# Performance work log

Measured on AMD Instinct MI355X. Metric: run time of the kernel, lower is better.

The kernel has to match this reference:

```python
import jax, jax.numpy as jnp
import numpy as np

N = 50000      # num nodes
IN = 256       # in_channels
H = 4          # heads
C = 64         # out_channels per head (concat=False -> out_dim = C)
HOPS = 3       # max_hops == num hops provided
E = 400000     # edges per hop
NEG_SLOPE = 0.2


def setup_inputs() -> dict:
    key = jax.random.key(0)
    ks = jax.random.split(key, 10)
    s_in = 1.0 / np.sqrt(IN)
    s_c = 1.0 / np.sqrt(C)
    return {
        "x": jax.random.normal(ks[0], (N, IN), jnp.float32),
        "ei0": jax.random.randint(ks[1], (2, E), 0, N, dtype=jnp.int32),
        "ei1": jax.random.randint(ks[2], (2, E), 0, N, dtype=jnp.int32),
        "ei2": jax.random.randint(ks[3], (2, E), 0, N, dtype=jnp.int32),
        # shared left/right projections (lin_l / lin_r, shared across hops)
        "W_l": jax.random.normal(ks[4], (IN, H * C), jnp.float32) * s_in,
        "b_l": jnp.zeros((H * C,), jnp.float32),
        "W_r": jax.random.normal(ks[5], (IN, H * C), jnp.float32) * s_in,
        "b_r": jnp.zeros((H * C,), jnp.float32),
        # hop-specific attention vectors and output biases
        "att": jax.random.normal(ks[6], (HOPS, H, C), jnp.float32) * s_c,
        "bias": jnp.zeros((HOPS, C), jnp.float32),
        # hop gate (single Linear since gate_hidden=None)
        "W_gate": jax.random.normal(ks[7], (IN, HOPS), jnp.float32) * s_in,
        "b_gate": jnp.zeros((HOPS,), jnp.float32),
    }


def _segment_softmax(logits, seg, n):
    # logits: [E, H], seg: [E] destination node ids
    m = jax.ops.segment_max(logits, seg, num_segments=n)          # [N, H]
    m = jnp.where(jnp.isfinite(m), m, 0.0)                        # empty segments -> 0
    ex = jnp.exp(logits - m[seg])
    s = jax.ops.segment_sum(ex, seg, num_segments=n)              # [N, H]
    return ex / (s[seg] + 1e-16)


def _gatv2_hop(x_l, x_r, edge_index, att_k, bias_k):
    # x_l, x_r: [N, H, C] shared projections; edge_index: [2, Ek]
    src, dst = edge_index[0], edge_index[1]
    s = jax.nn.leaky_relu(x_l[src] + x_r[dst], NEG_SLOPE)         # [Ek, H, C]
    alpha = jnp.einsum("ehc,hc->eh", s, att_k)                    # [Ek, H]
    alpha = _segment_softmax(alpha, dst, N)
    msg = jax.ops.segment_sum(x_l[src] * alpha[..., None], dst, num_segments=N)  # [N, H, C]
    return msg.mean(axis=1) + bias_k                              # concat=False -> head mean, [N, C]


def reference(x, ei0, ei1, ei2, W_l, b_l, W_r, b_r, att, bias, W_gate, b_gate):
    # shared projections computed once
    x_l = (x @ W_l + b_l).reshape(N, H, C)
    x_r = (x @ W_r + b_r).reshape(N, H, C)

    # hop 0 gets self-loops (add_self_loops=True); higher hops do not
    ar = jnp.arange(N, dtype=ei0.dtype)
    ei0_sl = jnp.concatenate([ei0, jnp.stack([ar, ar])], axis=1)
    edges = [ei0_sl, ei1, ei2]

    messages = jnp.stack(
        [_gatv2_hop(x_l, x_r, edges[k], att[k], bias[k]) for k in range(HOPS)],
        axis=1,
    )  # [N, HOPS, C]

    logits = x @ W_gate + b_gate                                  # [N, HOPS]
    weights = jax.nn.softmax(logits, axis=-1)
    out = jnp.einsum("nkc,nk->nc", messages, weights)             # [N, C]
    return out
```

## Files before the change

### kernel.cpp

```cpp
#include <hip/hip_runtime.h>
#include <math.h>

#define N_NODES 50000
#define IN_DIM 256
#define HEADS 4
#define CDIM 64
#define HC 256
#define HOPS 3
#define EDGES 400000
#define NEG_SLOPE 0.2f
#define SEG (EDGES + N_NODES)
#define TOT_E (3 * EDGES + N_NODES)
#define CAP 40

#define NB_GATE  ((N_NODES + 3) / 4)
#define NB_PACKW ((IN_DIM * 2 * HC) / 256)
#define NB_SCAT  ((TOT_E + 255) / 256)
#define GEMM_BX  ((N_NODES + 127) / 128)

typedef unsigned short ushort;
using short8  = __attribute__((ext_vector_type(8))) short;
using floatx4 = __attribute__((ext_vector_type(4))) float;

__device__ __forceinline__ void decode_flat(int f, int& k, int& e)
{
    if (f < SEG)              { k = 0; e = f; }
    else if (f < SEG + EDGES) { k = 1; e = f - SEG; }
    else                      { k = 2; e = f - SEG - EDGES; }
}

__device__ __forceinline__ ushort f2bf(float f)
{
    unsigned u = __float_as_uint(f);
    unsigned r = u + 0x7fffu + ((u >> 16) & 1u);
    return (ushort)(r >> 16);
}

__global__ __launch_bounds__(256) void prep(
    const float* __restrict__ X, const float* __restrict__ Wg,
    const float* __restrict__ bg, float* __restrict__ gw,
    ushort* __restrict__ Xb,
    const float* __restrict__ Wl, const float* __restrict__ Wr,
    ushort* __restrict__ WT,
    const int* __restrict__ ei0, const int* __restrict__ ei1,
    const int* __restrict__ ei2, int* __restrict__ cnt,
    int* __restrict__ bucket)
{
    const int blk = blockIdx.x;
    const int tid = threadIdx.x;

    if (blk < NB_GATE) {
        const int node = (blk * 256 + tid) >> 6;
        const int lane = tid & 63;
        if (node >= N_NODES) return;

        float4 xv = ((const float4*)(X + (size_t)node * IN_DIM))[lane];

        union { ushort s[4]; uint2 u; } o;
        o.s[0] = f2bf(xv.x); o.s[1] = f2bf(xv.y);
        o.s[2] = f2bf(xv.z); o.s[3] = f2bf(xv.w);
        ((uint2*)(Xb + (size_t)node * IN_DIM))[lane] = o.u;

        float a0 = 0.f, a1 = 0.f, a2 = 0.f;
        const int i0 = lane * 4;
        a0 += xv.x * Wg[(i0 + 0) * HOPS + 0]; a1 += xv.x * Wg[(i0 + 0) * HOPS + 1]; a2 += xv.x * Wg[(i0 + 0) * HOPS + 2];
        a0 += xv.y * Wg[(i0 + 1) * HOPS + 0]; a1 += xv.y * Wg[(i0 + 1) * HOPS + 1]; a2 += xv.y * Wg[(i0 + 1) * HOPS + 2];
        a0 += xv.z * Wg[(i0 + 2) * HOPS + 0]; a1 += xv.z * Wg[(i0 + 2) * HOPS + 1]; a2 += xv.z * Wg[(i0 + 2) * HOPS + 2];
        a0 += xv.w * Wg[(i0 + 3) * HOPS + 0]; a1 += xv.w * Wg[(i0 + 3) * HOPS + 1]; a2 += xv.w * Wg[(i0 + 3) * HOPS + 2];

        #pragma unroll
        for (int off = 32; off >= 1; off >>= 1) {
            a0 += __shfl_xor(a0, off);
            a1 += __shfl_xor(a1, off);
            a2 += __shfl_xor(a2, off);
        }
        if (lane == 0) {
            float l0 = a0 + bg[0], l1 = a1 + bg[1], l2 = a2 + bg[2];
            float m = fmaxf(l0, fmaxf(l1, l2));
            float e0 = expf(l0 - m), e1 = expf(l1 - m), e2 = expf(l2 - m);
            float inv = 1.f / (e0 + e1 + e2);
            gw[node * HOPS + 0] = e0 * inv;
            gw[node * HOPS + 1] = e1 * inv;
            gw[node * HOPS + 2] = e2 * inv;
        }
    } else if (blk < NB_GATE + NB_PACKW) {
        int id = (blk - NB_GATE) * 256 + tid;
        int n = id >> 8;
        int k = id & 255;
        float v = (n < HC) ? Wl[k * HC + n] : Wr[k * HC + (n - HC)];
        WT[(size_t)n * IN_DIM + k] = f2bf(v);
    } else {
        int f = (blk - NB_GATE - NB_PACKW) * 256 + tid;
        if (f >= TOT_E) return;
        int k, e; decode_flat(f, k, e);
        int s, d;
        if (k == 0 && e >= EDGES) { s = d = e - EDGES; }
        else {
            const int* ei = (k == 0) ? ei0 : (k == 1) ? ei1 : ei2;
            s = ei[e]; d = ei[EDGES + e];
        }
        int pos = atomicAdd(&cnt[k * N_NODES + d], 1);
        if (pos < CAP)
            bucket[((size_t)k * N_NODES + d) * CAP + pos] = s;
    }
}

#define TM 128
#define TN 128
#define TK 32
#define LDP 40

__global__ __launch_bounds__(256) void gemm_mfma(
    const ushort* __restrict__ Xb, const ushort* __restrict__ WT,
    const float* __restrict__ b_l, const float* __restrict__ b_r,
    ushort* __restrict__ xlb, ushort* __restrict__ xrb, int M)
{
    __shared__ ushort As[TM][LDP];
    __shared__ ushort Bs[TN][LDP];
    const int tid  = threadIdx.x;
    const int wave = tid >> 6, lane = tid & 63;
    const int row0 = blockIdx.x * TM;
    const int col0 = blockIdx.y * TN;
    const int wy = (wave >> 1) * 64, wx = (wave & 1) * 64;
    const int lrow = lane & 15, lk = (lane >> 4) * 8;

    floatx4 acc[4][4];
    #pragma unroll
    for (int i = 0; i < 4; i++)
        #pragma unroll
        for (int j = 0; j < 4; j++)
            acc[i][j] = (floatx4){0.f, 0.f, 0.f, 0.f};

    for (int k0 = 0; k0 < IN_DIM; k0 += TK) {
        #pragma unroll
        for (int j = 0; j < 2; j++) {
            int id = tid + 256 * j;
            int r  = id >> 2;
            int c  = (id & 3) * 8;
            int gr = row0 + r;
            uint4 v = make_uint4(0u, 0u, 0u, 0u);
            if (gr < M)
                v = *(const uint4*)(Xb + (size_t)gr * IN_DIM + k0 + c);
            *(uint4*)&As[r][c] = v;
        }
        #pragma unroll
        for (int j = 0; j < 2; j++) {
            int id = tid + 256 * j;
            int r  = id >> 2;
            int c  = (id & 3) * 8;
            *(uint4*)&Bs[r][c] =
                *(const uint4*)(WT + (size_t)(col0 + r) * IN_DIM + k0 + c);
        }
        __syncthreads();

        short8 af[4], bf[4];
        #pragma unroll
        for (int mi = 0; mi < 4; mi++)
            af[mi] = *(const short8*)&As[wy + mi * 16 + lrow][lk];
        #pragma unroll
        for (int ni = 0; ni < 4; ni++)
            bf[ni] = *(const short8*)&Bs[wx + ni * 16 + lrow][lk];

        #pragma unroll
        for (int mi = 0; mi < 4; mi++)
            #pragma unroll
            for (int ni = 0; ni < 4; ni++)
                acc[mi][ni] = __builtin_amdgcn_mfma_f32_16x16x32_bf16(
                    bf[ni], af[mi], acc[mi][ni], 0, 0, 0);
        __syncthreads();
    }

    const int csub = (lane >> 4) * 4;
    #pragma unroll
    for (int mi = 0; mi < 4; mi++) {
        int grow = row0 + wy + mi * 16 + lrow;
        if (grow < M) {
            #pragma unroll
            for (int ni = 0; ni < 4; ni++) {
                int gcol = col0 + wx + ni * 16 + csub;
                floatx4 v = acc[mi][ni];
                const bool left = (gcol < HC);
                const float4 b = left ? *(const float4*)(b_l + gcol)
                                      : *(const float4*)(b_r + gcol - HC);
                union { ushort s[4]; uint2 u; } o;
                o.s[0] = f2bf(v[0] + b.x);
                o.s[1] = f2bf(v[1] + b.y);
                o.s[2] = f2bf(v[2] + b.z);
                o.s[3] = f2bf(v[3] + b.w);
                ushort* dst = left ? (xlb + (size_t)grow * HC + gcol)
                                   : (xrb + (size_t)grow * HC + gcol - HC);
                *(uint2*)dst = o.u;
            }
        }
    }
}

__global__ __launch_bounds__(192) void node_all(
    const ushort* __restrict__ xlb, const ushort* __restrict__ xrb,
    const int* __restrict__ cnt, const int* __restrict__ bucket,
    const float* __restrict__ att, const float* __restrict__ gw,
    const float* __restrict__ bias, float* __restrict__ out)
{
    __shared__ float lds[HOPS][CDIM];
    const int n    = blockIdx.x;
    const int k    = threadIdx.x >> 6;
    const int lane = threadIdx.x & 63;
    const int half = lane >> 5;
    const int sub  = lane & 31;

    const int deg = min(cnt[k * N_NODES + n], CAP);
    const int* bk = bucket + ((size_t)k * N_NODES + n) * CAP;

    uint4 rq = *(const uint4*)(xrb + (size_t)n * HC + sub * 8);
    const float rr0 = __uint_as_float(rq.x << 16);
    const float rr1 = __uint_as_float(rq.x & 0xffff0000u);
    const float rr2 = __uint_as_float(rq.y << 16);
    const float rr3 = __uint_as_float(rq.y & 0xffff0000u);
    const float rr4 = __uint_as_float(rq.z << 16);
    const float rr5 = __uint_as_float(rq.z & 0xffff0000u);
    const float rr6 = __uint_as_float(rq.w << 16);
    const float rr7 = __uint_as_float(rq.w & 0xffff0000u);

    const float4 wa = ((const float4*)(att + (size_t)k * HC))[sub * 2 + 0];
    const float4 wb = ((const float4*)(att + (size_t)k * HC))[sub * 2 + 1];

    float denom = 0.f;
    float acc[8] = {0.f, 0.f, 0.f, 0.f, 0.f, 0.f, 0.f, 0.f};

    if (deg > 0) {
        int myS = (lane < deg) ? bk[lane] : 0;
        const int npair = (deg + 1) >> 1;

        int s0 = __shfl(myS, min(half, deg - 1));
        uint4 q = *(const uint4*)(xlb + (size_t)s0 * HC + sub * 8);

        for (int j = 0; j < npair; j++) {
            int idxn = min(2 * (j + 1) + half, deg - 1);
            int sn = __shfl(myS, idxn);
            uint4 qn = *(const uint4*)(xlb + (size_t)sn * HC + sub * 8);

            float f0 = __uint_as_float(q.x << 16);
            float f1 = __uint_as_float(q.x & 0xffff0000u);
            float f2 = __uint_as_float(q.y << 16);
            float f3 = __uint_as_float(q.y & 0xffff0000u);
            float f4 = __uint_as_float(q.z << 16);
            float f5 = __uint_as_float(q.z & 0xffff0000u);
            float f6 = __uint_as_float(q.w << 16);
            float f7 = __uint_as_float(q.w & 0xffff0000u);

            float v0 = f0 + rr0, v1 = f1 + rr1, v2 = f2 + rr2, v3 = f3 + rr3;
            float v4 = f4 + rr4, v5 = f5 + rr5, v6 = f6 + rr6, v7 = f7 + rr7;

            float p;
            p = 0.6f * wa.x * v0 + 0.4f * wa.x * fabsf(v0);
            p = fmaf(0.6f * wa.y, v1, p); p = fmaf(0.4f * wa.y, fabsf(v1), p);
            p = fmaf(0.6f * wa.z, v2, p); p = fmaf(0.4f * wa.z, fabsf(v2), p);
            p = fmaf(0.6f * wa.w, v3, p); p = fmaf(0.4f * wa.w, fabsf(v3), p);
            p = fmaf(0.6f * wb.x, v4, p); p = fmaf(0.4f * wb.x, fabsf(v4), p);
            p = fmaf(0.6f * wb.y, v5, p); p = fmaf(0.4f * wb.y, fabsf(v5), p);
            p = fmaf(0.6f * wb.z, v6, p); p = fmaf(0.4f * wb.z, fabsf(v6), p);
            p = fmaf(0.6f * wb.w, v7, p); p = fmaf(0.4f * wb.w, fabsf(v7), p);

            p += __shfl_xor(p, 1);
            p += __shfl_xor(p, 2);
            p += __shfl_xor(p, 4);

            bool valid = (2 * j + half) < deg;
            float ex = valid ? __expf(p) : 0.f;
            denom += ex;
            acc[0] = fmaf(ex, f0, acc[0]);
            acc[1] = fmaf(ex, f1, acc[1]);
            acc[2] = fmaf(ex, f2, acc[2]);
            acc[3] = fmaf(ex, f3, acc[3]);
            acc[4] = fmaf(ex, f4, acc[4]);
            acc[5] = fmaf(ex, f5, acc[5]);
            acc[6] = fmaf(ex, f6, acc[6]);
            acc[7] = fmaf(ex, f7, acc[7]);
            q = qn;
        }
    }

    denom += __shfl_xor(denom, 32);
    #pragma unroll
    for (int i = 0; i < 8; i++) acc[i] += __shfl_xor(acc[i], 32);

    float inv = (denom > 0.f) ? 1.f / denom : 0.f;
    const float g  = gw[n * HOPS + k];
    const float* bb = bias + (size_t)k * CDIM + (sub & 7) * 8;

    #pragma unroll
    for (int i = 0; i < 8; i++) {
        float v = acc[i] * inv;
        v += __shfl_xor(v, 8);
        v += __shfl_xor(v, 16);
        if (lane < 8) lds[k][lane * 8 + i] = g * (v * 0.25f + bb[i]);
    }
    __syncthreads();

    if (threadIdx.x < CDIM)
        out[(size_t)n * CDIM + threadIdx.x] =
            lds[0][threadIdx.x] + lds[1][threadIdx.x] + lds[2][threadIdx.x];
}

extern "C" void kernel_launch(void* const* d_in, const int* in_sizes, int n_in,
                              void* d_out, int out_size, void* d_ws, size_t ws_size,
                              hipStream_t stream)
{
    const float* x      = (const float*)d_in[0];
    const int*   ei0    = (const int*)d_in[1];
    const int*   ei1    = (const int*)d_in[2];
    const int*   ei2    = (const int*)d_in[3];
    const float* W_l    = (const float*)d_in[4];
    const float* b_l    = (const float*)d_in[5];
    const float* W_r    = (const float*)d_in[6];
    const float* b_r    = (const float*)d_in[7];
    const float* att    = (const float*)d_in[8];
    const float* bias   = (const float*)d_in[9];
    const float* W_gate = (const float*)d_in[10];
    const float* b_gate = (const float*)d_in[11];

    const size_t NHC = (size_t)N_NODES * HC;
    float* ws      = (float*)d_ws;
    float* gwbuf   = ws;
    int*   cnt     = (int*)(gwbuf + HOPS * N_NODES);
    int*   bucket  = cnt + HOPS * N_NODES;
    ushort* xlb    = (ushort*)(bucket + (size_t)HOPS * N_NODES * CAP);
    ushort* xrb    = xlb + NHC;
    ushort* Xb     = xrb + NHC;
    ushort* WT     = Xb + NHC;

    hipMemsetAsync(cnt, 0, (size_t)HOPS * N_NODES * sizeof(int), stream);

    prep<<<NB_GATE + NB_PACKW + NB_SCAT, 256, 0, stream>>>(
        x, W_gate, b_gate, gwbuf, Xb, W_l, W_r, WT,
        ei0, ei1, ei2, cnt, bucket);

    dim3 ggrid(GEMM_BX, 4);
    gemm_mfma<<<ggrid, 256, 0, stream>>>(Xb, WT, b_l, b_r, xlb, xrb, N_NODES);

    node_all<<<N_NODES, 192, 0, stream>>>(
        xlb, xrb, cnt, bucket, att, gwbuf, bias, (float*)d_out);
}
```

Measured before the change: 393.8 us.

## Process all hops per wave with packed float2 math, drop LDS reduction

The node aggregation kernel now assigns one wave per node and loops over the three hops serially inside that wave. Previously each node got a block of three waves, one per hop, combined through LDS and a barrier. Hop results are accumulated in registers and written directly with vector stores. Leaky-ReLU and the attention dot product are rewritten with packed two-wide float ops and an elementwise max. This removes the LDS and barrier cost and the tiny blocks, but each wave now runs its hops serially, which lowers memory-level parallelism per node.

```diff
diff --git a/kernel.cpp b/kernel.cpp
--- a/kernel.cpp
+++ b/kernel.cpp
@@ -21,6 +21,7 @@
 typedef unsigned short ushort;
 using short8  = __attribute__((ext_vector_type(8))) short;
 using floatx4 = __attribute__((ext_vector_type(4))) float;
+using f32x2   = __attribute__((ext_vector_type(2))) float;
 
 __device__ __forceinline__ void decode_flat(int f, int& k, int& e)
 {
@@ -34,6 +35,19 @@
     unsigned u = __float_as_uint(f);
     unsigned r = u + 0x7fffu + ((u >> 16) & 1u);
     return (ushort)(r >> 16);
+}
+
+__device__ __forceinline__ f32x2 bf2x(unsigned u)
+{
+    f32x2 r;
+    r.x = __uint_as_float(u << 16);
+    r.y = __uint_as_float(u & 0xffff0000u);
+    return r;
+}
+
+__device__ __forceinline__ f32x2 lrelu2(f32x2 v)
+{
+    return __builtin_elementwise_max(v, 0.2f * v);
 }
 
 __global__ __launch_bounds__(256) void prep(
@@ -195,111 +209,107 @@
     }
 }
 
-__global__ __launch_bounds__(192) void node_all(
+__global__ __launch_bounds__(256) void node_all(
     const ushort* __restrict__ xlb, const ushort* __restrict__ xrb,
     const int* __restrict__ cnt, const int* __restrict__ bucket,
     const float* __restrict__ att, const float* __restrict__ gw,
     const float* __restrict__ bias, float* __restrict__ out)
 {
-    __shared__ float lds[HOPS][CDIM];
-    const int n    = blockIdx.x;
-    const int k    = threadIdx.x >> 6;
+    const int n    = blockIdx.x * 4 + (threadIdx.x >> 6);
     const int lane = threadIdx.x & 63;
+    if (n >= N_NODES) return;
     const int half = lane >> 5;
     const int sub  = lane & 31;
-
-    const int deg = min(cnt[k * N_NODES + n], CAP);
-    const int* bk = bucket + ((size_t)k * N_NODES + n) * CAP;
-
-    uint4 rq = *(const uint4*)(xrb + (size_t)n * HC + sub * 8);
-    const float rr0 = __uint_as_float(rq.x << 16);
-    const float rr1 = __uint_as_float(rq.x & 0xffff0000u);
-    const float rr2 = __uint_as_float(rq.y << 16);
-    const float rr3 = __uint_as_float(rq.y & 0xffff0000u);
-    const float rr4 = __uint_as_float(rq.z << 16);
-    const float rr5 = __uint_as_float(rq.z & 0xffff0000u);
-    const float rr6 = __uint_as_float(rq.w << 16);
-    const float rr7 = __uint_as_float(rq.w & 0xffff0000u);
-
-    const float4 wa = ((const float4*)(att + (size_t)k * HC))[sub * 2 + 0];
-    const float4 wb = ((const float4*)(att + (size_t)k * HC))[sub * 2 + 1];
-
-    float denom = 0.f;
-    float acc[8] = {0.f, 0.f, 0.f, 0.f, 0.f, 0.f, 0.f, 0.f};
-
-    if (deg > 0) {
-        int myS = (lane < deg) ? bk[lane] : 0;
-        const int npair = (deg + 1) >> 1;
-
-        int s0 = __shfl(myS, min(half, deg - 1));
-        uint4 q = *(const uint4*)(xlb + (size_t)s0 * HC + sub * 8);
-
-        for (int j = 0; j < npair; j++) {
-            int idxn = min(2 * (j + 1) + half, deg - 1);
-            int sn = __shfl(myS, idxn);
-            uint4 qn = *(const uint4*)(xlb + (size_t)sn * HC + sub * 8);
-
-            float f0 = __uint_as_float(q.x << 16);
-            float f1 = __uint_as_float(q.x & 0xffff0000u);
-            float f2 = __uint_as_float(q.y << 16);
-            float f3 = __uint_as_float(q.y & 0xffff0000u);
-            float f4 = __uint_as_float(q.z << 16);
-            float f5 = __uint_as_float(q.z & 0xffff0000u);
-            float f6 = __uint_as_float(q.w << 16);
-            float f7 = __uint_as_float(q.w & 0xffff0000u);
-
-            float v0 = f0 + rr0, v1 = f1 + rr1, v2 = f2 + rr2, v3 = f3 + rr3;
-            float v4 = f4 + rr4, v5 = f5 + rr5, v6 = f6 + rr6, v7 = f7 + rr7;
-
-            float p;
-            p = 0.6f * wa.x * v0 + 0.4f * wa.x * fabsf(v0);
-            p = fmaf(0.6f * wa.y, v1, p); p = fmaf(0.4f * wa.y, fabsf(v1), p);
-            p = fmaf(0.6f * wa.z, v2, p); p = fmaf(0.4f * wa.z, fabsf(v2), p);
-            p = fmaf(0.6f * wa.w, v3, p); p = fmaf(0.4f * wa.w, fabsf(v3), p);
-            p = fmaf(0.6f * wb.x, v4, p); p = fmaf(0.4f * wb.x, fabsf(v4), p);
-            p = fmaf(0.6f * wb.y, v5, p); p = fmaf(0.4f * wb.y, fabsf(v5), p);
-            p = fmaf(0.6f * wb.z, v6, p); p = fmaf(0.4f * wb.z, fabsf(v6), p);
-            p = fmaf(0.6f * wb.w, v7, p); p = fmaf(0.4f * wb.w, fabsf(v7), p);
-
-            p += __shfl_xor(p, 1);
-            p += __shfl_xor(p, 2);
-            p += __shfl_xor(p, 4);
-
-            bool valid = (2 * j + half) < deg;
-            float ex = valid ? __expf(p) : 0.f;
-            denom += ex;
-            acc[0] = fmaf(ex, f0, acc[0]);
-            acc[1] = fmaf(ex, f1, acc[1]);
-            acc[2] = fmaf(ex, f2, acc[2]);
-            acc[3] = fmaf(ex, f3, acc[3]);
-            acc[4] = fmaf(ex, f4, acc[4]);
-            acc[5] = fmaf(ex, f5, acc[5]);
-            acc[6] = fmaf(ex, f6, acc[6]);
-            acc[7] = fmaf(ex, f7, acc[7]);
-            q = qn;
-        }
-    }
-
-    denom += __shfl_xor(denom, 32);
+    const unsigned laneoff = (unsigned)sub * 8;
+
+    uint4 rq = *(const uint4*)(xrb + (size_t)n * HC + laneoff);
+    f32x2 rr[4] = { bf2x(rq.x), bf2x(rq.y), bf2x(rq.z), bf2x(rq.w) };
+
+    f32x2 outacc[4] = { {0.f,0.f}, {0.f,0.f}, {0.f,0.f}, {0.f,0.f} };
+
     #pragma unroll
-    for (int i = 0; i < 8; i++) acc[i] += __shfl_xor(acc[i], 32);
-
-    float inv = (denom > 0.f) ? 1.f / denom : 0.f;
-    const float g  = gw[n * HOPS + k];
-    const float* bb = bias + (size_t)k * CDIM + (sub & 7) * 8;
-
-    #pragma unroll
-    for (int i = 0; i < 8; i++) {
-        float v = acc[i] * inv;
-        v += __shfl_xor(v, 8);
-        v += __shfl_xor(v, 16);
-        if (lane < 8) lds[k][lane * 8 + i] = g * (v * 0.25f + bb[i]);
-    }
-    __syncthreads();
-
-    if (threadIdx.x < CDIM)
-        out[(size_t)n * CDIM + threadIdx.x] =
-            lds[0][threadIdx.x] + lds[1][threadIdx.x] + lds[2][threadIdx.x];
+    for (int k = 0; k < HOPS; ++k) {
+        const int deg = min(cnt[k * N_NODES + n], CAP);
+        const int* bk = bucket + ((size_t)k * N_NODES + n) * CAP;
+
+        const float4 a0 = ((const float4*)(att + (size_t)k * HC))[sub * 2 + 0];
+        const float4 a1 = ((const float4*)(att + (size_t)k * HC))[sub * 2 + 1];
+        f32x2 w2[4] = { {a0.x, a0.y}, {a0.z, a0.w}, {a1.x, a1.y}, {a1.z, a1.w} };
+
+        float denom = 0.f;
+        f32x2 acc2[4] = { {0.f,0.f}, {0.f,0.f}, {0.f,0.f}, {0.f,0.f} };
+
+        if (deg > 0) {
+            const int degm1 = deg - 1;
+            int myS = (lane < deg) ? bk[lane] : 0;
+            const int npair = (deg + 1) >> 1;
+
+            int s0 = __shfl(myS, min(half, degm1));
+            uint4 q = *(const uint4*)(xlb + (unsigned)s0 * HC + laneoff);
+
+            for (int j = 0; j < npair; j++) {
+                int sn = __shfl(myS, min(2 * (j + 1) + half, degm1));
+                uint4 qn = *(const uint4*)(xlb + (unsigned)sn * HC + laneoff);
+
+                f32x2 f0 = bf2x(q.x), f1 = bf2x(q.y);
+                f32x2 f2 = bf2x(q.z), f3 = bf2x(q.w);
+
+                f32x2 pp = w2[0] * lrelu2(f0 + rr[0]);
+                pp = __builtin_elementwise_fma(w2[1], lrelu2(f1 + rr[1]), pp);
+                pp = __builtin_elementwise_fma(w2[2], lrelu2(f2 + rr[2]), pp);
+                pp = __builtin_elementwise_fma(w2[3], lrelu2(f3 + rr[3]), pp);
+                float p = pp.x + pp.y;
+
+                p += __shfl_xor(p, 1);
+                p += __shfl_xor(p, 2);
+                p += __shfl_xor(p, 4);
+
+                bool valid = (2 * j + half) < deg;
+                float ex = valid ? __expf(p) : 0.f;
+                denom += ex;
+                f32x2 ex2 = { ex, ex };
+                acc2[0] = __builtin_elementwise_fma(ex2, f0, acc2[0]);
+                acc2[1] = __builtin_elementwise_fma(ex2, f1, acc2[1]);
+                acc2[2] = __builtin_elementwise_fma(ex2, f2, acc2[2]);
+                acc2[3] = __builtin_elementwise_fma(ex2, f3, acc2[3]);
+                q = qn;
+            }
+        }
+
+        denom += __shfl_xor(denom, 32);
+        const float inv = (denom > 0.f) ? 1.f / denom : 0.f;
+        #pragma unroll
+        for (int i = 0; i < 4; i++) {
+            acc2[i].x += __shfl_xor(acc2[i].x, 32);
+            acc2[i].y += __shfl_xor(acc2[i].y, 32);
+            acc2[i].x *= inv;
+            acc2[i].y *= inv;
+            acc2[i].x += __shfl_xor(acc2[i].x, 8);
+            acc2[i].y += __shfl_xor(acc2[i].y, 8);
+            acc2[i].x += __shfl_xor(acc2[i].x, 16);
+            acc2[i].y += __shfl_xor(acc2[i].y, 16);
+        }
+
+        const float g   = gw[n * HOPS + k];
+        const float s   = g * 0.25f;
+        const f32x2 s2  = { s, s };
+        const f32x2 g2  = { g, g };
+        const f32x2* bb2 =
+            (const f32x2*)(bias + (size_t)k * CDIM + (size_t)(sub & 7) * 8);
+        #pragma unroll
+        for (int i = 0; i < 4; i++) {
+            outacc[i] = __builtin_elementwise_fma(s2, acc2[i], outacc[i]);
+            outacc[i] = __builtin_elementwise_fma(g2, bb2[i], outacc[i]);
+        }
+    }
+
+    if (lane < 8) {
+        float4 o0 = { outacc[0].x, outacc[0].y, outacc[1].x, outacc[1].y };
+        float4 o1 = { outacc[2].x, outacc[2].y, outacc[3].x, outacc[3].y };
+        float4* dst = (float4*)(out + (size_t)n * CDIM + (size_t)lane * 8);
+        dst[0] = o0;
+        dst[1] = o1;
+    }
 }
 
 extern "C" void kernel_launch(void* const* d_in, const int* in_sizes, int n_in,
@@ -338,6 +348,6 @@
     dim3 ggrid(GEMM_BX, 4);
     gemm_mfma<<<ggrid, 256, 0, stream>>>(Xb, WT, b_l, b_r, xlb, xrb, N_NODES);
 
-    node_all<<<N_NODES, 192, 0, stream>>>(
+    node_all<<<(N_NODES + 3) / 4, 256, 0, stream>>>(
         xlb, xrb, cnt, bucket, att, gwbuf, bias, (float*)d_out);
 }
```

After: 406.4 us. 1.03x slower.
